# Kernel optimization log

Hardware: AMD Instinct MI355X
Metric: run time of the kernel (lower is better)

The kernel has to match this reference:

```python
import jax, jax.numpy as jnp
import numpy as np

D_MODEL = 1024
NUM_HEADS = 16
D_K = D_MODEL // NUM_HEADS


def setup_inputs() -> dict:
    key = jax.random.key(0)
    ks = jax.random.split(key, 9)
    B, S = 4, 2048
    scale = 1.0 / np.sqrt(D_MODEL)
    x = jax.random.normal(ks[0], (B, S, D_MODEL), dtype=jnp.float32)
    wq = jax.random.normal(ks[1], (D_MODEL, D_MODEL), dtype=jnp.float32) * scale
    wk = jax.random.normal(ks[2], (D_MODEL, D_MODEL), dtype=jnp.float32) * scale
    wv = jax.random.normal(ks[3], (D_MODEL, D_MODEL), dtype=jnp.float32) * scale
    wo = jax.random.normal(ks[4], (D_MODEL, D_MODEL), dtype=jnp.float32) * scale
    bq = jax.random.normal(ks[5], (D_MODEL,), dtype=jnp.float32) * 0.01
    bk = jax.random.normal(ks[6], (D_MODEL,), dtype=jnp.float32) * 0.01
    bv = jax.random.normal(ks[7], (D_MODEL,), dtype=jnp.float32) * 0.01
    bo = jax.random.normal(ks[8], (D_MODEL,), dtype=jnp.float32) * 0.01
    return {"x": x, "wq": wq, "bq": bq, "wk": wk, "bk": bk,
            "wv": wv, "bv": bv, "wo": wo, "bo": bo}


def reference(x, wq, bq, wk, bk, wv, bv, wo, bo):
    B, S, _ = x.shape
    # projections -> [B, H, S, d_k]
    def split_heads(t):
        return t.reshape(B, S, NUM_HEADS, D_K).transpose(0, 2, 1, 3)
    q = split_heads(x @ wq.T + bq)
    k = split_heads(x @ wk.T + bk)
    v = split_heads(x @ wv.T + bv)
    scores = jnp.einsum("bhqd,bhkd->bhqk", q, k) / np.sqrt(D_K).astype(np.float32)
    attn = jax.nn.softmax(scores, axis=-1)  # dropout is identity at eval
    out = jnp.einsum("bhqk,bhkd->bhqd", attn, v)
    out = out.transpose(0, 2, 1, 3).reshape(B, S, D_MODEL)
    return out @ wo.T + bo
```

## Files before the change

### kernel.cpp

```cpp
#include <hip/hip_runtime.h>

#define D_MODEL 1024
#define NHEADS  16
#define DK      64
#define BATCH   4
#define SEQ     2048
#define MROWS   (BATCH*SEQ)
#define BHCOUNT (BATCH*NHEADS)

typedef _Float16 half8 __attribute__((ext_vector_type(8)));
typedef _Float16 half4 __attribute__((ext_vector_type(4)));
typedef float    floatx4 __attribute__((ext_vector_type(4)));
typedef float    floatx16 __attribute__((ext_vector_type(16)));

__device__ __forceinline__ void load_lds16(const void* g, void* l) {
    __builtin_amdgcn_global_load_lds((const __attribute__((address_space(1))) void*)g,
                                     (__attribute__((address_space(3))) void*)l, 16, 0, 0);
}

__device__ __forceinline__ unsigned pkrtz_u32(float a, float b) {
    auto h = __builtin_amdgcn_cvt_pkrtz(a, b);
    union { decltype(h) v; unsigned u; } c; c.v = h; return c.u;
}

__device__ __forceinline__ int permrow(int r) {
    return (r & ~12) | ((r & 4) << 1) | ((r & 8) >> 1);
}

__global__ __launch_bounds__(256)
void cvt_f32_f16(const float* __restrict__ in, _Float16* __restrict__ out) {
    size_t i = ((size_t)blockIdx.x*256 + threadIdx.x)*4;
    float4 v = *(const float4*)(in + i);
    half4 h = {(_Float16)v.x, (_Float16)v.y, (_Float16)v.z, (_Float16)v.w};
    *(half4*)(out + i) = h;
}

__global__ __launch_bounds__(256)
void cvt4_f32_f16(const float* __restrict__ a, const float* __restrict__ b,
                  const float* __restrict__ c, const float* __restrict__ d,
                  _Float16* __restrict__ oa, _Float16* __restrict__ ob,
                  _Float16* __restrict__ oc, _Float16* __restrict__ od) {
    const float* src; _Float16* dst;
    switch (blockIdx.y) {
        case 0:  src=a; dst=oa; break;
        case 1:  src=b; dst=ob; break;
        case 2:  src=c; dst=oc; break;
        default: src=d; dst=od; break;
    }
    size_t i = ((size_t)blockIdx.x*256 + threadIdx.x)*4;
    float4 v = *(const float4*)(src + i);
    half4 h = {(_Float16)v.x, (_Float16)v.y, (_Float16)v.z, (_Float16)v.w};
    *(half4*)(dst + i) = h;
}

template<int MODE>
__global__ __launch_bounds__(256)
void gemm_nt_f16(const _Float16* __restrict__ A, const _Float16* __restrict__ W,
                 const float* __restrict__ bias, void* __restrict__ Cout, float scale)
{
    __shared__ _Float16 As[2][128*32];
    __shared__ _Float16 Ws[2][128*32];
    const int t = threadIdx.x;
    const int w = t >> 6, l = t & 63;
    const int wm = w >> 1, wn = w & 1;
    const int bm = blockIdx.y*128, bn = blockIdx.x*128;
    const int lrow = l & 15, lq4 = l >> 4;
    const int xc = (lq4 ^ ((lrow >> 1) & 3)) * 8;

    int srow[2], scol[2];
    #pragma unroll
    for (int it = 0; it < 2; ++it) {
        int s = (it*4 + w)*64 + l;
        int r = s >> 2;
        int lc = (s & 3) ^ ((r >> 1) & 3);
        srow[it] = r; scol[it] = lc*8;
    }

    floatx4 acc[4][4];
    #pragma unroll
    for (int i = 0; i < 4; ++i)
        #pragma unroll
        for (int j = 0; j < 4; ++j) acc[i][j] = (floatx4){0.f,0.f,0.f,0.f};

    #pragma unroll
    for (int it = 0; it < 2; ++it) {
        load_lds16(A + (size_t)(bm + srow[it])*1024 + scol[it], &As[0][(it*4+w)*512]);
        load_lds16(W + (size_t)(bn + srow[it])*1024 + scol[it], &Ws[0][(it*4+w)*512]);
    }

    for (int kt = 0; kt < 32; ++kt) {
        __syncthreads();
        const int cur = kt & 1;
        if (kt + 1 < 32) {
            const int k1 = (kt + 1)*32;
            #pragma unroll
            for (int it = 0; it < 2; ++it) {
                load_lds16(A + (size_t)(bm + srow[it])*1024 + k1 + scol[it], &As[cur^1][(it*4+w)*512]);
                load_lds16(W + (size_t)(bn + srow[it])*1024 + k1 + scol[it], &Ws[cur^1][(it*4+w)*512]);
            }
        }
        half8 af[4], bf[4];
        #pragma unroll
        for (int i = 0; i < 4; ++i) af[i] = *(half8*)&As[cur][(wm*64 + i*16 + lrow)*32 + xc];
        #pragma unroll
        for (int j = 0; j < 4; ++j) bf[j] = *(half8*)&Ws[cur][(wn*64 + j*16 + lrow)*32 + xc];
        #pragma unroll
        for (int i = 0; i < 4; ++i)
            #pragma unroll
            for (int j = 0; j < 4; ++j)
                acc[i][j] = __builtin_amdgcn_mfma_f32_16x16x32_f16(af[i], bf[j], acc[i][j], 0, 0, 0);
    }

    #pragma unroll
    for (int j = 0; j < 4; ++j) {
        int gcol = bn + wn*64 + j*16 + lrow;
        float bv = bias[gcol];
        #pragma unroll
        for (int i = 0; i < 4; ++i) {
            #pragma unroll
            for (int r = 0; r < 4; ++r) {
                int gm = bm + wm*64 + i*16 + lq4*4 + r;
                float val = (acc[i][j][r] + bv) * scale;
                if (MODE == 0) {
                    ((float*)Cout)[(size_t)gm*1024 + gcol] = val;
                } else {
                    int b = gm >> 11, s = gm & 2047;
                    int h = gcol >> 6, dk = gcol & 63;
                    ((_Float16*)Cout)[(((size_t)(b*NHEADS + h))*SEQ + s)*DK + dk] = (_Float16)val;
                }
            }
        }
    }
}

__global__ __launch_bounds__(256)
void transpose_v(const _Float16* __restrict__ V, _Float16* __restrict__ Vt)
{
    __shared__ unsigned Lt[64][33];
    const int t = threadIdx.x;
    const int bh = blockIdx.y;
    const int s0 = blockIdx.x*64;
    const _Float16* Vb = V + ((size_t)bh*SEQ + s0)*DK;
    const int sp = t >> 3, dkc = (t & 7)*8;
    uint4 r0 = *(const uint4*)(Vb + (2*sp+0)*64 + dkc);
    uint4 r1 = *(const uint4*)(Vb + (2*sp+1)*64 + dkc);
    unsigned a0[4] = {r0.x, r0.y, r0.z, r0.w};
    unsigned a1[4] = {r1.x, r1.y, r1.z, r1.w};
    #pragma unroll
    for (int i = 0; i < 4; ++i) {
        Lt[dkc+2*i+0][sp] = (a0[i] & 0xFFFFu) | (a1[i] << 16);
        Lt[dkc+2*i+1][sp] = (a0[i] >> 16)     | (a1[i] & 0xFFFF0000u);
    }
    __syncthreads();
    const int dk = t >> 2, spc = (t & 3)*8;
    uint4 o0 = {Lt[dk][spc+0], Lt[dk][spc+1], Lt[dk][spc+2], Lt[dk][spc+3]};
    uint4 o1 = {Lt[dk][spc+4], Lt[dk][spc+5], Lt[dk][spc+6], Lt[dk][spc+7]};
    _Float16* dst = Vt + ((size_t)bh*DK + dk)*SEQ + s0 + spc*2;
    *(uint4*)(dst)     = o0;
    *(uint4*)(dst + 8) = o1;
}

__global__ __launch_bounds__(256)
void attn_mfma(const _Float16* __restrict__ Q, const _Float16* __restrict__ K,
               const _Float16* __restrict__ Vt, _Float16* __restrict__ AO)
{
    __shared__ _Float16 Ks[2][64*64];
    __shared__ _Float16 Vs[2][64*64];

    const int t = threadIdx.x;
    const int w = t >> 6, l = t & 63;
    const int l31 = l & 31, hi = l >> 5;
    const int bh = blockIdx.y;
    const int q0 = blockIdx.x*128;

    const _Float16* Qb = Q  + ((size_t)bh*SEQ + q0)*DK;
    const _Float16* Kb = K  + (size_t)bh*SEQ*DK;
    const _Float16* Vb = Vt + (size_t)bh*DK*SEQ;

    int srow[2], scol[2], karow[2];
    #pragma unroll
    for (int it = 0; it < 2; ++it) {
        int s = (it*4 + w)*64 + l;
        int r = s >> 3;
        int lc = (s & 7) ^ (r & 7);
        srow[it] = r; scol[it] = lc*8;
        karow[it] = permrow(r);
    }

    half8 qf[4];
    #pragma unroll
    for (int kk = 0; kk < 4; ++kk)
        qf[kk] = *(const half8*)(Qb + (size_t)(w*32 + l31)*DK + kk*16 + hi*8);

    #pragma unroll
    for (int it = 0; it < 2; ++it) {
        load_lds16(Kb + (size_t)karow[it]*DK + scol[it], &Ks[0][(it*4+w)*512]);
        load_lds16(Vb + (size_t)srow[it]*SEQ + scol[it], &Vs[0][(it*4+w)*512]);
    }

    floatx16 Oacc[2];
    #pragma unroll
    for (int n = 0; n < 2; ++n)
        #pragma unroll
        for (int i = 0; i < 16; ++i) Oacc[n][i] = 0.f;
    float psum = 0.f;

    for (int kt = 0; kt < SEQ/64; ++kt) {
        __syncthreads();
        const int cur = kt & 1;
        if (kt + 1 < SEQ/64) {
            #pragma unroll
            for (int it = 0; it < 2; ++it) {
                load_lds16(Kb + ((size_t)((kt+1)*64 + karow[it]))*DK + scol[it], &Ks[cur^1][(it*4+w)*512]);
                load_lds16(Vb + (size_t)srow[it]*SEQ + (kt+1)*64 + scol[it],    &Vs[cur^1][(it*4+w)*512]);
            }
        }

        #pragma unroll
        for (int kb = 0; kb < 2; ++kb) {
            floatx16 sT;
            #pragma unroll
            for (int i = 0; i < 16; ++i) sT[i] = 0.f;
            #pragma unroll
            for (int kk = 0; kk < 4; ++kk) {
                int row = kb*32 + l31;
                half8 kf = *(half8*)&Ks[cur][row*64 + (((kk*2 + hi) ^ (row & 7)))*8];
                sT = __builtin_amdgcn_mfma_f32_32x32x16_f16(kf, qf[kk], sT, 0, 0, 0);
            }

            unsigned Wd[8];
            #pragma unroll
            for (int p = 0; p < 8; ++p) {
                float p0 = exp2f(sT[2*p]);
                float p1 = exp2f(sT[2*p+1]);
                psum += p0 + p1;
                Wd[p] = pkrtz_u32(p0, p1);
            }

            #pragma unroll
            for (int kk2 = 0; kk2 < 2; ++kk2) {
                union { unsigned u[4]; half8 h; } pf;
                #pragma unroll
                for (int v = 0; v < 4; ++v) pf.u[v] = Wd[kk2*4 + v];
                #pragma unroll
                for (int n = 0; n < 2; ++n) {
                    int vrow = n*32 + l31;
                    int vg = kb*4 + kk2*2 + hi;
                    half8 vf = *(half8*)&Vs[cur][vrow*64 + ((vg ^ (vrow & 7)))*8];
                    Oacc[n] = __builtin_amdgcn_mfma_f32_32x32x16_f16(pf.h, vf, Oacc[n], 0, 0, 0);
                }
            }
        }
    }

    float lsum = psum + __shfl_xor(psum, 32, 64);
    float inv = 1.f / lsum;

    float invr[16];
    #pragma unroll
    for (int r = 0; r < 16; ++r)
        invr[r] = __shfl(inv, (r & 3) + 8*(r >> 2) + 4*hi, 64);

    const int b = bh >> 4, h = bh & 15;
    #pragma unroll
    for (int n = 0; n < 2; ++n)
        #pragma unroll
        for (int r = 0; r < 16; ++r) {
            int qrow = (r & 3) + 8*(r >> 2) + 4*hi;
            int gq = q0 + w*32 + qrow;
            AO[((size_t)(b*SEQ + gq))*D_MODEL + h*DK + n*32 + l31] =
                (_Float16)(Oacc[n][r] * invr[r]);
        }
}

extern "C" void kernel_launch(void* const* d_in, const int* in_sizes, int n_in,
                              void* d_out, int out_size, void* d_ws, size_t ws_size,
                              hipStream_t stream)
{
    const float* x  = (const float*)d_in[0];
    const float* wq = (const float*)d_in[1];
    const float* bq = (const float*)d_in[2];
    const float* wk = (const float*)d_in[3];
    const float* bk = (const float*)d_in[4];
    const float* wv = (const float*)d_in[5];
    const float* bv = (const float*)d_in[6];
    const float* wo = (const float*)d_in[7];
    const float* bo = (const float*)d_in[8];

    const size_t NX = (size_t)MROWS * D_MODEL;
    const size_t NW = (size_t)D_MODEL * D_MODEL;
    _Float16* xh  = (_Float16*)d_ws;
    _Float16* wqh = xh  + NX;
    _Float16* wkh = wqh + NW;
    _Float16* wvh = wkh + NW;
    _Float16* woh = wvh + NW;
    _Float16* Qh  = woh + NW;
    _Float16* Kh  = Qh  + NX;
    _Float16* Vh  = Kh  + NX;
    _Float16* Vth = Vh  + NX;
    _Float16* AOh = Vth + NX;

    cvt_f32_f16<<<NX/1024, 256, 0, stream>>>(x, xh);
    cvt4_f32_f16<<<dim3(NW/1024, 4), 256, 0, stream>>>(wq, wk, wv, wo, wqh, wkh, wvh, woh);

    const float QSCALE = 0.125f * 1.44269504f;
    dim3 pgrid(D_MODEL/128, MROWS/128);
    gemm_nt_f16<1><<<pgrid, 256, 0, stream>>>(xh, wqh, bq, Qh, QSCALE);
    gemm_nt_f16<1><<<pgrid, 256, 0, stream>>>(xh, wkh, bk, Kh, 1.0f);
    gemm_nt_f16<1><<<pgrid, 256, 0, stream>>>(xh, wvh, bv, Vh, 1.0f);

    transpose_v<<<dim3(SEQ/64, BHCOUNT), 256, 0, stream>>>(Vh, Vth);
    attn_mfma<<<dim3(SEQ/128, BHCOUNT), 256, 0, stream>>>(Qh, Kh, Vth, AOh);

    gemm_nt_f16<0><<<pgrid, 256, 0, stream>>>(AOh, woh, bo, d_out, 1.0f);
}
```

Measured before the change: 362.5 us.

## Give each attention wave two query tiles and compute row sums via MFMA

The attention block drops from 4 to 2 waves. Each wave now owns 64 query rows as two 32-row tiles, so every K and V fragment read from LDS feeds two MFMAs. The softmax denominator is no longer a scalar psum plus shuffles; it is accumulated by an extra MFMA of P against a ones vector. The step is manually unrolled over the two LDS buffers and uses the raw exp2 intrinsic. The aim is to halve LDS reads per MFMA and remove VALU reduction work, at the cost of more accumulator registers and fewer waves per block to hide latency.

```diff
diff --git a/kernel.cpp b/kernel.cpp
--- a/kernel.cpp
+++ b/kernel.cpp
@@ -7,6 +7,7 @@
 #define SEQ     2048
 #define MROWS   (BATCH*SEQ)
 #define BHCOUNT (BATCH*NHEADS)
+#define KTILES  (SEQ/64)
 
 typedef _Float16 half8 __attribute__((ext_vector_type(8)));
 typedef _Float16 half4 __attribute__((ext_vector_type(4)));
@@ -160,7 +161,7 @@
     *(uint4*)(dst + 8) = o1;
 }
 
-__global__ __launch_bounds__(256)
+__global__ __launch_bounds__(128)
 void attn_mfma(const _Float16* __restrict__ Q, const _Float16* __restrict__ K,
                const _Float16* __restrict__ Vt, _Float16* __restrict__ AO)
 {
@@ -177,99 +178,122 @@
     const _Float16* Kb = K  + (size_t)bh*SEQ*DK;
     const _Float16* Vb = Vt + (size_t)bh*DK*SEQ;
 
-    int srow[2], scol[2], karow[2];
-    #pragma unroll
-    for (int it = 0; it < 2; ++it) {
-        int s = (it*4 + w)*64 + l;
+    int srow[4], scol[4], karow[4];
+    #pragma unroll
+    for (int it = 0; it < 4; ++it) {
+        int s = (it*2 + w)*64 + l;
         int r = s >> 3;
         int lc = (s & 7) ^ (r & 7);
         srow[it] = r; scol[it] = lc*8;
         karow[it] = permrow(r);
     }
 
-    half8 qf[4];
-    #pragma unroll
-    for (int kk = 0; kk < 4; ++kk)
-        qf[kk] = *(const half8*)(Qb + (size_t)(w*32 + l31)*DK + kk*16 + hi*8);
-
-    #pragma unroll
-    for (int it = 0; it < 2; ++it) {
-        load_lds16(Kb + (size_t)karow[it]*DK + scol[it], &Ks[0][(it*4+w)*512]);
-        load_lds16(Vb + (size_t)srow[it]*SEQ + scol[it], &Vs[0][(it*4+w)*512]);
-    }
-
-    floatx16 Oacc[2];
-    #pragma unroll
-    for (int n = 0; n < 2; ++n)
-        #pragma unroll
-        for (int i = 0; i < 16; ++i) Oacc[n][i] = 0.f;
-    float psum = 0.f;
-
-    for (int kt = 0; kt < SEQ/64; ++kt) {
-        __syncthreads();
-        const int cur = kt & 1;
-        if (kt + 1 < SEQ/64) {
-            #pragma unroll
-            for (int it = 0; it < 2; ++it) {
-                load_lds16(Kb + ((size_t)((kt+1)*64 + karow[it]))*DK + scol[it], &Ks[cur^1][(it*4+w)*512]);
-                load_lds16(Vb + (size_t)srow[it]*SEQ + (kt+1)*64 + scol[it],    &Vs[cur^1][(it*4+w)*512]);
-            }
-        }
-
-        #pragma unroll
-        for (int kb = 0; kb < 2; ++kb) {
-            floatx16 sT;
-            #pragma unroll
-            for (int i = 0; i < 16; ++i) sT[i] = 0.f;
-            #pragma unroll
-            for (int kk = 0; kk < 4; ++kk) {
-                int row = kb*32 + l31;
-                half8 kf = *(half8*)&Ks[cur][row*64 + (((kk*2 + hi) ^ (row & 7)))*8];
-                sT = __builtin_amdgcn_mfma_f32_32x32x16_f16(kf, qf[kk], sT, 0, 0, 0);
-            }
-
-            unsigned Wd[8];
-            #pragma unroll
-            for (int p = 0; p < 8; ++p) {
-                float p0 = exp2f(sT[2*p]);
-                float p1 = exp2f(sT[2*p+1]);
-                psum += p0 + p1;
-                Wd[p] = pkrtz_u32(p0, p1);
-            }
-
-            #pragma unroll
-            for (int kk2 = 0; kk2 < 2; ++kk2) {
-                union { unsigned u[4]; half8 h; } pf;
-                #pragma unroll
-                for (int v = 0; v < 4; ++v) pf.u[v] = Wd[kk2*4 + v];
-                #pragma unroll
-                for (int n = 0; n < 2; ++n) {
-                    int vrow = n*32 + l31;
-                    int vg = kb*4 + kk2*2 + hi;
-                    half8 vf = *(half8*)&Vs[cur][vrow*64 + ((vg ^ (vrow & 7)))*8];
-                    Oacc[n] = __builtin_amdgcn_mfma_f32_32x32x16_f16(pf.h, vf, Oacc[n], 0, 0, 0);
-                }
-            }
-        }
-    }
-
-    float lsum = psum + __shfl_xor(psum, 32, 64);
-    float inv = 1.f / lsum;
-
-    float invr[16];
-    #pragma unroll
-    for (int r = 0; r < 16; ++r)
-        invr[r] = __shfl(inv, (r & 3) + 8*(r >> 2) + 4*hi, 64);
+    half8 qf[2][4];
+    #pragma unroll
+    for (int qt = 0; qt < 2; ++qt)
+        #pragma unroll
+        for (int kk = 0; kk < 4; ++kk)
+            qf[qt][kk] = *(const half8*)(Qb + (size_t)(w*64 + qt*32 + l31)*DK + kk*16 + hi*8);
+
+    #pragma unroll
+    for (int it = 0; it < 4; ++it) {
+        load_lds16(Kb + (size_t)karow[it]*DK + scol[it], &Ks[0][(it*2+w)*512]);
+        load_lds16(Vb + (size_t)srow[it]*SEQ + scol[it], &Vs[0][(it*2+w)*512]);
+    }
+
+    floatx16 Oacc[2][2];
+    floatx16 lacc[2];
+    #pragma unroll
+    for (int qt = 0; qt < 2; ++qt) {
+        #pragma unroll
+        for (int i = 0; i < 16; ++i) { Oacc[qt][0][i] = 0.f; Oacc[qt][1][i] = 0.f; lacc[qt][i] = 0.f; }
+    }
+    floatx16 z16;
+    #pragma unroll
+    for (int i = 0; i < 16; ++i) z16[i] = 0.f;
+    half8 onesf;
+    #pragma unroll
+    for (int i = 0; i < 8; ++i) onesf[i] = (_Float16)1.f;
+
+#define ATTN_PREFETCH(NBUF, KT1)                                                          \
+    if ((KT1) < KTILES) {                                                                 \
+        _Pragma("unroll")                                                                 \
+        for (int it = 0; it < 4; ++it) {                                                  \
+            load_lds16(Kb + ((size_t)((KT1)*64 + karow[it]))*DK + scol[it],               \
+                       &Ks[NBUF][(it*2+w)*512]);                                          \
+            load_lds16(Vb + (size_t)srow[it]*SEQ + (KT1)*64 + scol[it],                   \
+                       &Vs[NBUF][(it*2+w)*512]);                                          \
+        }                                                                                 \
+    }
+
+#define ATTN_STEP(CUR, KT)                                                                \
+    {                                                                                     \
+        __syncthreads();                                                                  \
+        ATTN_PREFETCH((CUR)^1, (KT)+1)                                                    \
+        _Pragma("unroll")                                                                 \
+        for (int kb = 0; kb < 2; ++kb) {                                                  \
+            const int row = kb*32 + l31;                                                  \
+                                \
+            floatx16 sTa, sTb;                                                            \
+            {                                                                             \
+                half8 kf = *(half8*)&Ks[CUR][row*64 + ((hi ^ (row & 7)))*8];              \
+                sTa = __builtin_amdgcn_mfma_f32_32x32x16_f16(kf, qf[0][0], z16, 0, 0, 0); \
+                sTb = __builtin_amdgcn_mfma_f32_32x32x16_f16(kf, qf[1][0], z16, 0, 0, 0); \
+            }                                                                             \
+            _Pragma("unroll")                                                             \
+            for (int kk = 1; kk < 4; ++kk) {                                              \
+                half8 kf = *(half8*)&Ks[CUR][row*64 + (((kk*2 + hi) ^ (row & 7)))*8];     \
+                sTa = __builtin_amdgcn_mfma_f32_32x32x16_f16(kf, qf[0][kk], sTa, 0, 0, 0);\
+                sTb = __builtin_amdgcn_mfma_f32_32x32x16_f16(kf, qf[1][kk], sTb, 0, 0, 0);\
+            }                                                                             \
+                     \
+            unsigned Wda[8], Wdb[8];                                                      \
+            _Pragma("unroll")                                                             \
+            for (int p = 0; p < 8; ++p) {                                                 \
+                Wda[p] = pkrtz_u32(__builtin_amdgcn_exp2f(sTa[2*p]),                      \
+                                   __builtin_amdgcn_exp2f(sTa[2*p+1]));                   \
+                Wdb[p] = pkrtz_u32(__builtin_amdgcn_exp2f(sTb[2*p]),                      \
+                                   __builtin_amdgcn_exp2f(sTb[2*p+1]));                   \
+            }                                                                             \
+                                     \
+            _Pragma("unroll")                                                             \
+            for (int kk2 = 0; kk2 < 2; ++kk2) {                                           \
+                union { unsigned u[4]; half8 h; } pfa, pfb;                               \
+                _Pragma("unroll")                                                         \
+                for (int v = 0; v < 4; ++v) { pfa.u[v] = Wda[kk2*4 + v];                  \
+                                              pfb.u[v] = Wdb[kk2*4 + v]; }                \
+                lacc[0] = __builtin_amdgcn_mfma_f32_32x32x16_f16(pfa.h, onesf, lacc[0], 0, 0, 0); \
+                lacc[1] = __builtin_amdgcn_mfma_f32_32x32x16_f16(pfb.h, onesf, lacc[1], 0, 0, 0); \
+                const int vg = kb*4 + kk2*2 + hi;                                         \
+                _Pragma("unroll")                                                         \
+                for (int n = 0; n < 2; ++n) {                                             \
+                    const int vrow = n*32 + l31;                                          \
+                    half8 vf = *(half8*)&Vs[CUR][vrow*64 + ((vg ^ (vrow & 7)))*8];        \
+                    Oacc[0][n] = __builtin_amdgcn_mfma_f32_32x32x16_f16(pfa.h, vf, Oacc[0][n], 0, 0, 0); \
+                    Oacc[1][n] = __builtin_amdgcn_mfma_f32_32x32x16_f16(pfb.h, vf, Oacc[1][n], 0, 0, 0); \
+                }                                                                         \
+            }                                                                             \
+        }                                                                                 \
+    }
+
+    for (int ktp = 0; ktp < KTILES; ktp += 2) {
+        ATTN_STEP(0, ktp)
+        ATTN_STEP(1, ktp+1)
+    }
+#undef ATTN_STEP
+#undef ATTN_PREFETCH
 
     const int b = bh >> 4, h = bh & 15;
     #pragma unroll
-    for (int n = 0; n < 2; ++n)
+    for (int qt = 0; qt < 2; ++qt)
         #pragma unroll
         for (int r = 0; r < 16; ++r) {
+            float inv = 1.f / lacc[qt][r];
             int qrow = (r & 3) + 8*(r >> 2) + 4*hi;
-            int gq = q0 + w*32 + qrow;
-            AO[((size_t)(b*SEQ + gq))*D_MODEL + h*DK + n*32 + l31] =
-                (_Float16)(Oacc[n][r] * invr[r]);
+            int gq = q0 + w*64 + qt*32 + qrow;
+            _Float16* dst = AO + ((size_t)(b*SEQ + gq))*D_MODEL + h*DK;
+            dst[l31]      = (_Float16)(Oacc[qt][0][r] * inv);
+            dst[32 + l31] = (_Float16)(Oacc[qt][1][r] * inv);
         }
 }
 
@@ -310,7 +334,7 @@
     gemm_nt_f16<1><<<pgrid, 256, 0, stream>>>(xh, wvh, bv, Vh, 1.0f);
 
     transpose_v<<<dim3(SEQ/64, BHCOUNT), 256, 0, stream>>>(Vh, Vth);
-    attn_mfma<<<dim3(SEQ/128, BHCOUNT), 256, 0, stream>>>(Qh, Kh, Vth, AOh);
+    attn_mfma<<<dim3(SEQ/128, BHCOUNT), 128, 0, stream>>>(Qh, Kh, Vth, AOh);
 
     gemm_nt_f16<0><<<pgrid, 256, 0, stream>>>(AOh, woh, bo, d_out, 1.0f);
 }
```

After: 336.3 us. 1.08x faster.
